# Performance work log

Measured on AMD Instinct MI355X. Metric: run time of the kernel, lower is better.

Reference implementation:

```python
import jax, jax.numpy as jnp
import numpy as np

N_HEAD = 16
NEG = -10000.0


def setup_inputs() -> dict:
    key = jax.random.key(0)
    k1, k2, k3 = jax.random.split(key, 3)
    B, S, NX = 2, 2048, 1024
    x = jax.random.normal(k1, (B, S, NX), dtype=jnp.float32)
    # Conv1D weights: y = x @ W + b (HF Conv1D stores weight as [in, out])
    w_attn = jax.random.normal(k2, (NX, 3 * NX), dtype=jnp.float32) * 0.02
    b_attn = jnp.zeros((3 * NX,), dtype=jnp.float32)
    w_proj = jax.random.normal(k3, (NX, NX), dtype=jnp.float32) * 0.02
    b_proj = jnp.zeros((NX,), dtype=jnp.float32)
    return {"x": x, "w_attn": w_attn, "b_attn": b_attn,
            "w_proj": w_proj, "b_proj": b_proj}


def reference(x, w_attn, b_attn, w_proj, b_proj):
    B, S, NX = x.shape
    H = N_HEAD
    D = NX // H  # head dim
    qkv = x @ w_attn + b_attn                      # [B, S, 3*NX]
    q, k, v = jnp.split(qkv, 3, axis=-1)
    # split heads -> [B, H, S, D]
    q = q.reshape(B, S, H, D).transpose(0, 2, 1, 3)
    k = k.reshape(B, S, H, D).transpose(0, 2, 1, 3)
    v = v.reshape(B, S, H, D).transpose(0, 2, 1, 3)
    # scores [B, H, S, S], scaled (scale=True)
    w = jnp.einsum('bhqd,bhkd->bhqk', q, k) / jnp.sqrt(jnp.asarray(D, x.dtype))
    # causal additive mask exactly as the torch code: w*b + NEG*(1-b)
    bias = jnp.tril(jnp.ones((S, S), dtype=x.dtype))[None, None]  # [1,1,S,S]
    w = w * bias + NEG * (1.0 - bias)
    w = jax.nn.softmax(w, axis=-1)
    a = jnp.einsum('bhqk,bhkd->bhqd', w, v)        # [B, H, S, D]
    a = a.transpose(0, 2, 1, 3).reshape(B, S, NX)  # merge heads
    return a @ w_proj + b_proj
```

## Files before the change

### kernel.cpp

```cpp
#include <hip/hip_runtime.h>
#include <cstdint>
#include <cstddef>


typedef __bf16 bf16;
typedef __bf16 bf16x8 __attribute__((ext_vector_type(8)));
typedef __bf16 bf16x4 __attribute__((ext_vector_type(4)));
typedef float f32x4 __attribute__((ext_vector_type(4)));

#define MFMA16(a, b, c) __builtin_amdgcn_mfma_f32_16x16x32_bf16(a, b, c, 0, 0, 0)

typedef const __attribute__((address_space(1))) void* gas_ptr;
typedef __attribute__((address_space(3))) void* las_ptr;
__device__ __forceinline__ void async16(const void* g, void* l) {
    __builtin_amdgcn_global_load_lds((gas_ptr)g, (las_ptr)l, 16, 0, 0);
}
__device__ __forceinline__ float exp2f_fast(float x) { return __builtin_amdgcn_exp2f(x); }

__global__ void cvt_kernel(const float* __restrict__ in, bf16* __restrict__ out, int n) {
    int i = (blockIdx.x * blockDim.x + threadIdx.x) * 4;
    if (i >= n) return;
    float4 v = *reinterpret_cast<const float4*>(in + i);
    bf16x4 o;
    o[0] = (bf16)v.x; o[1] = (bf16)v.y; o[2] = (bf16)v.z; o[3] = (bf16)v.w;
    *reinterpret_cast<bf16x4*>(out + i) = o;
}

__global__ void transpose_kernel(const float* __restrict__ in, bf16* __restrict__ out,
                                 int K, int N) {
    __shared__ float tile[32][33];
    int n0 = blockIdx.x * 32, k0 = blockIdx.y * 32;
    int tx = threadIdx.x, ty = threadIdx.y;
#pragma unroll
    for (int i = 0; i < 32; i += 8)
        tile[ty + i][tx] = in[(size_t)(k0 + ty + i) * N + n0 + tx];
    __syncthreads();
#pragma unroll
    for (int i = 0; i < 32; i += 8)
        out[(size_t)(n0 + ty + i) * K + k0 + tx] = (bf16)tile[tx][ty + i];
}

template <int OUT_BF16>
__global__ __launch_bounds__(256) void gemm_kernel(const bf16* __restrict__ A,
                                                   const bf16* __restrict__ Bt,
                                                   const float* __restrict__ bias,
                                                   void* __restrict__ Cout,
                                                   int M, int N, int K) {
    __shared__ bf16 Alds[2][128 * 32];
    __shared__ bf16 Blds[2][128 * 32];
    const int tid = threadIdx.x;
    const int w = tid >> 6, l = tid & 63;
    const int lane16 = l & 15, quad = l >> 4;
    const int wr = w >> 1, wc = w & 1;
    const int row0 = blockIdx.y * 128, col0 = blockIdx.x * 128;

    const int e = tid * 8;
    const int sr = e >> 5, sc = e & 31;

    f32x4 zero4 = {0.f, 0.f, 0.f, 0.f};
    f32x4 acc[4][4];
#pragma unroll
    for (int i = 0; i < 4; ++i)
#pragma unroll
        for (int j = 0; j < 4; ++j) acc[i][j] = zero4;

#pragma unroll
    for (int ch = 0; ch < 2; ++ch) {
        async16(A + (size_t)(row0 + ch * 64 + sr) * K + sc, &Alds[0][ch * 2048 + e]);
        async16(Bt + (size_t)(col0 + ch * 64 + sr) * K + sc, &Blds[0][ch * 2048 + e]);
    }

    const int niter = K >> 5;
    for (int it = 0; it < niter; ++it) {
        const int cur = it & 1;
        __syncthreads();
        if (it + 1 < niter) {
            const int k1 = (it + 1) << 5;
#pragma unroll
            for (int ch = 0; ch < 2; ++ch) {
                async16(A + (size_t)(row0 + ch * 64 + sr) * K + k1 + sc, &Alds[cur ^ 1][ch * 2048 + e]);
                async16(Bt + (size_t)(col0 + ch * 64 + sr) * K + k1 + sc, &Blds[cur ^ 1][ch * 2048 + e]);
            }
        }
        bf16x8 af[4], bfr[4];
#pragma unroll
        for (int i = 0; i < 4; ++i) {
            af[i] = *reinterpret_cast<const bf16x8*>(&Alds[cur][(64 * wr + 16 * i + lane16) * 32 + quad * 8]);
            bfr[i] = *reinterpret_cast<const bf16x8*>(&Blds[cur][(64 * wc + 16 * i + lane16) * 32 + quad * 8]);
        }
#pragma unroll
        for (int i = 0; i < 4; ++i)
#pragma unroll
            for (int j = 0; j < 4; ++j) acc[i][j] = MFMA16(af[i], bfr[j], acc[i][j]);
    }

#pragma unroll
    for (int i = 0; i < 4; ++i)
#pragma unroll
        for (int j = 0; j < 4; ++j)
#pragma unroll
            for (int r = 0; r < 4; ++r) {
                int row = row0 + 64 * wr + 16 * i + quad * 4 + r;
                int col = col0 + 64 * wc + 16 * j + lane16;
                float v = acc[i][j][r] + bias[col];
                if (OUT_BF16)
                    reinterpret_cast<bf16*>(Cout)[(size_t)row * N + col] = (bf16)v;
                else
                    reinterpret_cast<float*>(Cout)[(size_t)row * N + col] = v;
            }
}

template <int OUT_BF16>
__global__ __launch_bounds__(256) void gemm64_kernel(const bf16* __restrict__ A,
                                                     const bf16* __restrict__ Bt,
                                                     const float* __restrict__ bias,
                                                     void* __restrict__ Cout,
                                                     int M, int N, int K) {
    __shared__ bf16 Alds[2][64 * 32];
    __shared__ bf16 Blds[2][128 * 32];
    const int tid = threadIdx.x;
    const int w = tid >> 6, l = tid & 63;
    const int lane16 = l & 15, quad = l >> 4;
    const int wr = w >> 1, wc = w & 1;
    const int row0 = blockIdx.y * 64, col0 = blockIdx.x * 128;

    const int e = tid * 8;
    const int sr = e >> 5, sc = e & 31;

    f32x4 zero4 = {0.f, 0.f, 0.f, 0.f};
    f32x4 acc[2][4];
#pragma unroll
    for (int i = 0; i < 2; ++i)
#pragma unroll
        for (int j = 0; j < 4; ++j) acc[i][j] = zero4;

    async16(A + (size_t)(row0 + sr) * K + sc, &Alds[0][e]);
#pragma unroll
    for (int ch = 0; ch < 2; ++ch)
        async16(Bt + (size_t)(col0 + ch * 64 + sr) * K + sc, &Blds[0][ch * 2048 + e]);

    const int niter = K >> 5;
    for (int it = 0; it < niter; ++it) {
        const int cur = it & 1;
        __syncthreads();
        if (it + 1 < niter) {
            const int k1 = (it + 1) << 5;
            async16(A + (size_t)(row0 + sr) * K + k1 + sc, &Alds[cur ^ 1][e]);
#pragma unroll
            for (int ch = 0; ch < 2; ++ch)
                async16(Bt + (size_t)(col0 + ch * 64 + sr) * K + k1 + sc, &Blds[cur ^ 1][ch * 2048 + e]);
        }
        bf16x8 af[2], bfr[4];
#pragma unroll
        for (int i = 0; i < 2; ++i)
            af[i] = *reinterpret_cast<const bf16x8*>(&Alds[cur][(32 * wr + 16 * i + lane16) * 32 + quad * 8]);
#pragma unroll
        for (int j = 0; j < 4; ++j)
            bfr[j] = *reinterpret_cast<const bf16x8*>(&Blds[cur][(64 * wc + 16 * j + lane16) * 32 + quad * 8]);
#pragma unroll
        for (int i = 0; i < 2; ++i)
#pragma unroll
            for (int j = 0; j < 4; ++j) acc[i][j] = MFMA16(af[i], bfr[j], acc[i][j]);
    }

#pragma unroll
    for (int i = 0; i < 2; ++i)
#pragma unroll
        for (int j = 0; j < 4; ++j)
#pragma unroll
            for (int r = 0; r < 4; ++r) {
                int row = row0 + 32 * wr + 16 * i + quad * 4 + r;
                int col = col0 + 64 * wc + 16 * j + lane16;
                float v = acc[i][j][r] + bias[col];
                if (OUT_BF16)
                    reinterpret_cast<bf16*>(Cout)[(size_t)row * N + col] = (bf16)v;
                else
                    reinterpret_cast<float*>(Cout)[(size_t)row * N + col] = v;
            }
}

__global__ __launch_bounds__(256) void attn_kernel(const bf16* __restrict__ qkv,
                                                   bf16* __restrict__ aout) {
    const int S = 2048;
    const int bh = blockIdx.x;
    const int b = bh >> 4, h = bh & 15;
    const int qt = 31 - blockIdx.y;
    const int nkt = qt + 1;
    const int tid = threadIdx.x, w = tid >> 6, l = tid & 63;
    const int lane16 = l & 15, quad = l >> 4;

    __shared__ bf16 Klds[64 * 72];
    __shared__ bf16 Vt[64 * 72];
    __shared__ bf16 Plds[4][16 * 72];

    const bf16* base = qkv + (size_t)b * S * 3072;
    const float qscale = 0.125f * 1.4426950408889634f;
    const float NEGs = -10000.0f * 1.4426950408889634f;

    bf16x8 qf[2];
#pragma unroll
    for (int hv = 0; hv < 2; ++hv) {
        const bf16* qp = base + (size_t)(qt * 64 + 16 * w + lane16) * 3072 + h * 64;
        bf16x8 t = *reinterpret_cast<const bf16x8*>(qp + hv * 32 + quad * 8);
#pragma unroll
        for (int j = 0; j < 8; ++j) t[j] = (bf16)((float)t[j] * qscale);
        qf[hv] = t;
    }

    f32x4 zero4 = {0.f, 0.f, 0.f, 0.f};
    f32x4 o[4];
#pragma unroll
    for (int df = 0; df < 4; ++df) o[df] = zero4;
    float lsum = 0.f;

    const int kr = tid >> 3, kc = (tid & 7) * 8;
    const int vp = tid & 31, vd = (tid >> 5) * 8;
    bf16x8 kreg0, kreg1, vreg0, vreg1;
    auto load_tile = [&](int kt) {
        const bf16* tb = base + (size_t)(kt * 64) * 3072;
        kreg0 = *reinterpret_cast<const bf16x8*>(tb + (size_t)kr * 3072 + 1024 + h * 64 + kc);
        kreg1 = *reinterpret_cast<const bf16x8*>(tb + (size_t)(32 + kr) * 3072 + 1024 + h * 64 + kc);
        vreg0 = *reinterpret_cast<const bf16x8*>(tb + (size_t)(2 * vp) * 3072 + 2048 + h * 64 + vd);
        vreg1 = *reinterpret_cast<const bf16x8*>(tb + (size_t)(2 * vp + 1) * 3072 + 2048 + h * 64 + vd);
    };

    load_tile(0);
    for (int kt = 0; kt < nkt; ++kt) {
        __syncthreads();
        *reinterpret_cast<bf16x8*>(&Klds[kr * 72 + kc]) = kreg0;
        *reinterpret_cast<bf16x8*>(&Klds[(32 + kr) * 72 + kc]) = kreg1;
#pragma unroll
        for (int j = 0; j < 8; ++j) {
            union { bf16 h2[2]; uint32_t u; } pk;
            pk.h2[0] = vreg0[j]; pk.h2[1] = vreg1[j];
            *reinterpret_cast<uint32_t*>(&Vt[(vd + j) * 72 + 2 * vp]) = pk.u;
        }
        __syncthreads();
        if (kt + 1 < nkt) load_tile(kt + 1);

        f32x4 st[4];
#pragma unroll
        for (int kf = 0; kf < 4; ++kf) {
            bf16x8 k0 = *reinterpret_cast<const bf16x8*>(&Klds[(kf * 16 + lane16) * 72 + quad * 8]);
            bf16x8 k1 = *reinterpret_cast<const bf16x8*>(&Klds[(kf * 16 + lane16) * 72 + 32 + quad * 8]);
            f32x4 z = zero4;
            z = MFMA16(k0, qf[0], z);
            z = MFMA16(k1, qf[1], z);
            st[kf] = z;
        }

        if (kt == qt) {
            const int q = qt * 64 + 16 * w + lane16;
#pragma unroll
            for (int kf = 0; kf < 4; ++kf)
#pragma unroll
                for (int r = 0; r < 4; ++r)
                    if (kt * 64 + kf * 16 + quad * 4 + r > q) st[kf][r] = NEGs;
        }

        float rs = 0.f;
        bf16* Prow = &Plds[w][lane16 * 72];
#pragma unroll
        for (int kf = 0; kf < 4; ++kf) {
            bf16x4 pk;
#pragma unroll
            for (int r = 0; r < 4; ++r) {
                float pv = exp2f_fast(st[kf][r]);
                rs += pv;
                pk[r] = (bf16)pv;
            }
            *reinterpret_cast<bf16x4*>(Prow + kf * 16 + quad * 4) = pk;
        }
        lsum += rs;

#pragma unroll
        for (int kf2 = 0; kf2 < 2; ++kf2) {
            bf16x8 pf = *reinterpret_cast<const bf16x8*>(
                &Plds[w][lane16 * 72 + kf2 * 32 + quad * 8]);
#pragma unroll
            for (int df = 0; df < 4; ++df) {
                bf16x8 vf = *reinterpret_cast<const bf16x8*>(
                    &Vt[(df * 16 + lane16) * 72 + kf2 * 32 + quad * 8]);
                o[df] = MFMA16(pf, vf, o[df]);
            }
        }
    }

    lsum += __shfl_xor(lsum, 16, 64);
    lsum += __shfl_xor(lsum, 32, 64);
    float inv = 1.0f / lsum;

#pragma unroll
    for (int r = 0; r < 4; ++r) {
        float li = __shfl(inv, quad * 4 + r, 64);
        int row = qt * 64 + 16 * w + quad * 4 + r;
#pragma unroll
        for (int df = 0; df < 4; ++df)
            aout[(size_t)(b * S + row) * 1024 + h * 64 + df * 16 + lane16] =
                (bf16)(o[df][r] * li);
    }
}

extern "C" void kernel_launch(void* const* d_in, const int* in_sizes, int n_in,
                              void* d_out, int out_size, void* d_ws, size_t ws_size,
                              hipStream_t stream) {
    const float* x      = (const float*)d_in[0];
    const float* w_attn = (const float*)d_in[1];
    const float* b_attn = (const float*)d_in[2];
    const float* w_proj = (const float*)d_in[3];
    const float* b_proj = (const float*)d_in[4];
    float* out = (float*)d_out;
    char* ws = (char*)d_ws;

    const int Mtok = 4096, NX = 1024, N3 = 3072;
    bf16* xb   = (bf16*)(ws);
    bf16* wTa  = (bf16*)(ws + ((size_t)8 << 20));
    bf16* wTp  = (bf16*)(ws + ((size_t)14 << 20));
    bf16* qkv  = (bf16*)(ws + ((size_t)16 << 20));
    bf16* abuf = (bf16*)(ws + ((size_t)40 << 20));

    cvt_kernel<<<dim3((Mtok * NX / 4 + 255) / 256), 256, 0, stream>>>(x, xb, Mtok * NX);
    transpose_kernel<<<dim3(N3 / 32, NX / 32), dim3(32, 8), 0, stream>>>(w_attn, wTa, NX, N3);
    transpose_kernel<<<dim3(NX / 32, NX / 32), dim3(32, 8), 0, stream>>>(w_proj, wTp, NX, NX);

    gemm_kernel<1><<<dim3(N3 / 128, Mtok / 128), 256, 0, stream>>>(xb, wTa, b_attn, qkv, Mtok, N3, NX);
    attn_kernel<<<dim3(32, 32), 256, 0, stream>>>(qkv, abuf);
    gemm64_kernel<0><<<dim3(NX / 128, Mtok / 64), 256, 0, stream>>>(abuf, wTp, b_proj, out, Mtok, NX, NX);
}
```

Baseline: 178.3 us.

## Process 128-query tiles per attention block and fuse prep kernels into one launch

The attention kernel now gives each block 128 query rows, two 16-row fragments per wave, so every K/V tile staged in LDS feeds twice as many queries. Grid y shrinks to 16 and is ordered to interleave long and short causal blocks. Fragments that lie wholly above the diagonal skip their MFMAs. Separately, the bf16 conversion of x and the two weight transposes are merged into one launch. This halves attention block count (512 blocks), which may hurt occupancy and load balance, and raises register pressure.

```diff
diff --git a/kernel.cpp b/kernel.cpp
--- a/kernel.cpp
+++ b/kernel.cpp
@@ -17,20 +17,25 @@
 }
 __device__ __forceinline__ float exp2f_fast(float x) { return __builtin_amdgcn_exp2f(x); }
 
-__global__ void cvt_kernel(const float* __restrict__ in, bf16* __restrict__ out, int n) {
-    int i = (blockIdx.x * blockDim.x + threadIdx.x) * 4;
-    if (i >= n) return;
-    float4 v = *reinterpret_cast<const float4*>(in + i);
-    bf16x4 o;
-    o[0] = (bf16)v.x; o[1] = (bf16)v.y; o[2] = (bf16)v.z; o[3] = (bf16)v.w;
-    *reinterpret_cast<bf16x4*>(out + i) = o;
-}
-
-__global__ void transpose_kernel(const float* __restrict__ in, bf16* __restrict__ out,
-                                 int K, int N) {
+__global__ __launch_bounds__(256) void prep_kernel(const float* __restrict__ x, bf16* __restrict__ xb,
+                                                   const float* __restrict__ wa, bf16* __restrict__ wTa,
+                                                   const float* __restrict__ wp, bf16* __restrict__ wTp) {
     __shared__ float tile[32][33];
-    int n0 = blockIdx.x * 32, k0 = blockIdx.y * 32;
-    int tx = threadIdx.x, ty = threadIdx.y;
+    const int bid = blockIdx.x, tid = threadIdx.x;
+    if (bid < 4096) {
+        int i = (bid * 256 + tid) * 4;
+        float4 v = *reinterpret_cast<const float4*>(x + i);
+        bf16x4 o;
+        o[0] = (bf16)v.x; o[1] = (bf16)v.y; o[2] = (bf16)v.z; o[3] = (bf16)v.w;
+        *reinterpret_cast<bf16x4*>(xb + i) = o;
+        return;
+    }
+    const float* in; bf16* out; int N, t;
+    if (bid < 7168) { t = bid - 4096; in = wa; out = wTa; N = 3072; }
+    else            { t = bid - 7168; in = wp; out = wTp; N = 1024; }
+    const int K = 1024;
+    int bx = t % (N >> 5), by = t / (N >> 5);
+    int n0 = bx * 32, k0 = by * 32, tx = tid & 31, ty = tid >> 5;
 #pragma unroll
     for (int i = 0; i < 32; i += 8)
         tile[ty + i][tx] = in[(size_t)(k0 + ty + i) * N + n0 + tx];
@@ -184,34 +189,41 @@
     const int S = 2048;
     const int bh = blockIdx.x;
     const int b = bh >> 4, h = bh & 15;
-    const int qt = 31 - blockIdx.y;
-    const int nkt = qt + 1;
+    const int y = blockIdx.y;
+    const int qb = (y < 8) ? (15 - y) : (y - 8);
+    const int nkt = 2 * qb + 2;
     const int tid = threadIdx.x, w = tid >> 6, l = tid & 63;
     const int lane16 = l & 15, quad = l >> 4;
+    const int qw0 = qb * 128 + 32 * w;
 
     __shared__ bf16 Klds[64 * 72];
     __shared__ bf16 Vt[64 * 72];
-    __shared__ bf16 Plds[4][16 * 72];
+    __shared__ bf16 Plds[4][2][16 * 72];
 
     const bf16* base = qkv + (size_t)b * S * 3072;
     const float qscale = 0.125f * 1.4426950408889634f;
     const float NEGs = -10000.0f * 1.4426950408889634f;
 
-    bf16x8 qf[2];
-#pragma unroll
-    for (int hv = 0; hv < 2; ++hv) {
-        const bf16* qp = base + (size_t)(qt * 64 + 16 * w + lane16) * 3072 + h * 64;
-        bf16x8 t = *reinterpret_cast<const bf16x8*>(qp + hv * 32 + quad * 8);
-#pragma unroll
-        for (int j = 0; j < 8; ++j) t[j] = (bf16)((float)t[j] * qscale);
-        qf[hv] = t;
+    bf16x8 qf[2][2];
+#pragma unroll
+    for (int rf = 0; rf < 2; ++rf) {
+        const bf16* qp = base + (size_t)(qw0 + 16 * rf + lane16) * 3072 + h * 64;
+#pragma unroll
+        for (int hv = 0; hv < 2; ++hv) {
+            bf16x8 t = *reinterpret_cast<const bf16x8*>(qp + hv * 32 + quad * 8);
+#pragma unroll
+            for (int j = 0; j < 8; ++j) t[j] = (bf16)((float)t[j] * qscale);
+            qf[rf][hv] = t;
+        }
     }
 
     f32x4 zero4 = {0.f, 0.f, 0.f, 0.f};
-    f32x4 o[4];
-#pragma unroll
-    for (int df = 0; df < 4; ++df) o[df] = zero4;
-    float lsum = 0.f;
+    f32x4 o[2][4];
+#pragma unroll
+    for (int rf = 0; rf < 2; ++rf)
+#pragma unroll
+        for (int df = 0; df < 4; ++df) o[rf][df] = zero4;
+    float lsum[2] = {0.f, 0.f};
 
     const int kr = tid >> 3, kc = (tid & 7) * 8;
     const int vp = tid & 31, vd = (tid >> 5) * 8;
@@ -238,66 +250,87 @@
         __syncthreads();
         if (kt + 1 < nkt) load_tile(kt + 1);
 
-        f32x4 st[4];
+        const bool act0 = (kt * 64 <= qw0 + 15);
+        const bool act1 = (kt * 64 <= qw0 + 31);
+        if (!act1) continue;
+
+        f32x4 st[2][4];
 #pragma unroll
         for (int kf = 0; kf < 4; ++kf) {
             bf16x8 k0 = *reinterpret_cast<const bf16x8*>(&Klds[(kf * 16 + lane16) * 72 + quad * 8]);
             bf16x8 k1 = *reinterpret_cast<const bf16x8*>(&Klds[(kf * 16 + lane16) * 72 + 32 + quad * 8]);
             f32x4 z = zero4;
-            z = MFMA16(k0, qf[0], z);
-            z = MFMA16(k1, qf[1], z);
-            st[kf] = z;
-        }
-
-        if (kt == qt) {
-            const int q = qt * 64 + 16 * w + lane16;
-#pragma unroll
-            for (int kf = 0; kf < 4; ++kf)
-#pragma unroll
-                for (int r = 0; r < 4; ++r)
-                    if (kt * 64 + kf * 16 + quad * 4 + r > q) st[kf][r] = NEGs;
-        }
-
-        float rs = 0.f;
-        bf16* Prow = &Plds[w][lane16 * 72];
-#pragma unroll
-        for (int kf = 0; kf < 4; ++kf) {
-            bf16x4 pk;
-#pragma unroll
-            for (int r = 0; r < 4; ++r) {
-                float pv = exp2f_fast(st[kf][r]);
-                rs += pv;
-                pk[r] = (bf16)pv;
-            }
-            *reinterpret_cast<bf16x4*>(Prow + kf * 16 + quad * 4) = pk;
-        }
-        lsum += rs;
+            z = MFMA16(k0, qf[1][0], z);
+            z = MFMA16(k1, qf[1][1], z);
+            st[1][kf] = z;
+            if (act0) {
+                z = zero4;
+                z = MFMA16(k0, qf[0][0], z);
+                z = MFMA16(k1, qf[0][1], z);
+                st[0][kf] = z;
+            }
+        }
+
+#pragma unroll
+        for (int rf = 0; rf < 2; ++rf) {
+            if (rf == 0 && !act0) continue;
+            if (kt * 64 + 63 > qw0 + 16 * rf) {
+                const int q = qw0 + 16 * rf + lane16;
+#pragma unroll
+                for (int kf = 0; kf < 4; ++kf)
+#pragma unroll
+                    for (int r = 0; r < 4; ++r)
+                        if (kt * 64 + kf * 16 + quad * 4 + r > q) st[rf][kf][r] = NEGs;
+            }
+            float rs = 0.f;
+            bf16* Prow = &Plds[w][rf][lane16 * 72];
+#pragma unroll
+            for (int kf = 0; kf < 4; ++kf) {
+                bf16x4 pk;
+#pragma unroll
+                for (int r = 0; r < 4; ++r) {
+                    float pv = exp2f_fast(st[rf][kf][r]);
+                    rs += pv;
+                    pk[r] = (bf16)pv;
+                }
+                *reinterpret_cast<bf16x4*>(Prow + kf * 16 + quad * 4) = pk;
+            }
+            lsum[rf] += rs;
+        }
 
 #pragma unroll
         for (int kf2 = 0; kf2 < 2; ++kf2) {
-            bf16x8 pf = *reinterpret_cast<const bf16x8*>(
-                &Plds[w][lane16 * 72 + kf2 * 32 + quad * 8]);
+            bf16x8 pf1 = *reinterpret_cast<const bf16x8*>(
+                &Plds[w][1][lane16 * 72 + kf2 * 32 + quad * 8]);
+            bf16x8 pf0;
+            if (act0)
+                pf0 = *reinterpret_cast<const bf16x8*>(
+                    &Plds[w][0][lane16 * 72 + kf2 * 32 + quad * 8]);
 #pragma unroll
             for (int df = 0; df < 4; ++df) {
                 bf16x8 vf = *reinterpret_cast<const bf16x8*>(
                     &Vt[(df * 16 + lane16) * 72 + kf2 * 32 + quad * 8]);
-                o[df] = MFMA16(pf, vf, o[df]);
-            }
-        }
-    }
-
-    lsum += __shfl_xor(lsum, 16, 64);
-    lsum += __shfl_xor(lsum, 32, 64);
-    float inv = 1.0f / lsum;
-
-#pragma unroll
-    for (int r = 0; r < 4; ++r) {
-        float li = __shfl(inv, quad * 4 + r, 64);
-        int row = qt * 64 + 16 * w + quad * 4 + r;
-#pragma unroll
-        for (int df = 0; df < 4; ++df)
-            aout[(size_t)(b * S + row) * 1024 + h * 64 + df * 16 + lane16] =
-                (bf16)(o[df][r] * li);
+                o[1][df] = MFMA16(pf1, vf, o[1][df]);
+                if (act0) o[0][df] = MFMA16(pf0, vf, o[0][df]);
+            }
+        }
+    }
+
+#pragma unroll
+    for (int rf = 0; rf < 2; ++rf) {
+        float ls = lsum[rf];
+        ls += __shfl_xor(ls, 16, 64);
+        ls += __shfl_xor(ls, 32, 64);
+        float inv = 1.0f / ls;
+#pragma unroll
+        for (int r = 0; r < 4; ++r) {
+            float li = __shfl(inv, quad * 4 + r, 64);
+            int row = qw0 + 16 * rf + quad * 4 + r;
+#pragma unroll
+            for (int df = 0; df < 4; ++df)
+                aout[(size_t)(b * S + row) * 1024 + h * 64 + df * 16 + lane16] =
+                    (bf16)(o[rf][df][r] * li);
+        }
     }
 }
 
@@ -319,11 +352,8 @@
     bf16* qkv  = (bf16*)(ws + ((size_t)16 << 20));
     bf16* abuf = (bf16*)(ws + ((size_t)40 << 20));
 
-    cvt_kernel<<<dim3((Mtok * NX / 4 + 255) / 256), 256, 0, stream>>>(x, xb, Mtok * NX);
-    transpose_kernel<<<dim3(N3 / 32, NX / 32), dim3(32, 8), 0, stream>>>(w_attn, wTa, NX, N3);
-    transpose_kernel<<<dim3(NX / 32, NX / 32), dim3(32, 8), 0, stream>>>(w_proj, wTp, NX, NX);
-
+    prep_kernel<<<dim3(8192), 256, 0, stream>>>(x, xb, w_attn, wTa, w_proj, wTp);
     gemm_kernel<1><<<dim3(N3 / 128, Mtok / 128), 256, 0, stream>>>(xb, wTa, b_attn, qkv, Mtok, N3, NX);
-    attn_kernel<<<dim3(32, 32), 256, 0, stream>>>(qkv, abuf);
+    attn_kernel<<<dim3(32, 16), 256, 0, stream>>>(qkv, abuf);
     gemm64_kernel<0><<<dim3(NX / 128, Mtok / 64), 256, 0, stream>>>(abuf, wTp, b_proj, out, Mtok, NX, NX);
 }
```

Result: slower. 185.6 us (+4.1%).
